# Optimization experiments

Measured on AMD Instinct MI355X. Metric: run time of the kernel, lower is better.

## Reference

```python
import jax, jax.numpy as jnp
import numpy as np

MAX_DISP = 64  # init kwarg max_disp; feature_similarity='correlation'


def setup_inputs() -> dict:
    key = jax.random.key(0)
    k1, k2 = jax.random.split(key)
    shape = (8, 160, 320, 128)  # (b, h, w, c)
    left = jax.random.normal(k1, shape, dtype=jnp.float32)
    right = jax.random.normal(k2, shape, dtype=jnp.float32)
    return {"left_feature": left, "right_feature": right}


def reference(left_feature, right_feature):
    # Faithful to CostVolume.__call__ with feature_similarity='correlation':
    # cost[b,h,j,i] = mean_c( left[b,h,j,c] * right[b,h,j-i,c] ) for j >= i, else 0.
    b, h, w, c = left_feature.shape
    widx = jnp.arange(w)  # (w,)
    slices = []
    for i in range(MAX_DISP):  # fixed hyperparameter unroll, not a data dim
        # roll brings right[..., j-i, :] to position j along width; wrapped
        # positions j < i are masked to zero (original leaves them at init 0).
        corr = jnp.mean(left_feature * jnp.roll(right_feature, i, axis=2), axis=3)  # (b,h,w)
        corr = jnp.where(widx >= i, corr, jnp.zeros((), corr.dtype))
        slices.append(corr)
    return jnp.stack(slices, axis=-1)  # (b, h, w, max_disp)
```

## Files before the change

### kernel.cpp

```cpp
#include <hip/hip_runtime.h>

#define W  320
#define TJ 64

typedef __attribute__((ext_vector_type(8))) short   short8;
typedef __attribute__((ext_vector_type(4))) float   floatx4;

__device__ __forceinline__ unsigned int f2bf(float f) {
    unsigned int u = __float_as_uint(f);
    u += 0x7FFFu + ((u >> 16) & 1u);
    return u >> 16;
}

__global__ __launch_bounds__(512, 8)
void cost_volume_kernel(const float* __restrict__ Lg,
                        const float* __restrict__ Rg,
                        float* __restrict__ out) {
    __shared__ unsigned short S[128 * 128];

    const int lin  = blockIdx.x;
    const int work = (lin & 7) * 800 + (lin >> 3);
    const int bh   = work / 5;
    const int jt   = work - bh * 5;
    const int j0   = jt * TJ;
    const int tid  = threadIdx.x;

    const int lr    = tid >> 5;
    const int half  = tid & 1;
    const int chunk = (tid & 31) >> 1;
    const int cf    = (tid & 31) << 2;

    const int wave = tid >> 6;
    const int lane = tid & 63;
    const int col  = lane & 15;
    const int quad = lane >> 4;
    const int mt   = wave >> 1;
    const int g    = wave & 1;
    const int m0   = mt * 16;
    const int ntb  = mt + g * 3;
    const int NT   = g ? 2 : 3;

    const float* Rrow0 = Rg + (size_t)(bh * W) * 128;
    #pragma unroll
    for (int p = 0; p < 8; ++p) {
        const int rr = p * 16 + lr;
        const int k  = j0 - 63 + rr;
        floatx4 v;
        v.x = 0.f; v.y = 0.f; v.z = 0.f; v.w = 0.f;
        if (k >= 0 && k < W) v = *(const floatx4*)(Rrow0 + (size_t)k * 128 + cf);
        uint2 d;
        d.x = f2bf(v.x) | (f2bf(v.y) << 16);
        d.y = f2bf(v.z) | (f2bf(v.w) << 16);
        const int sw = chunk ^ (rr & 15);
        *(uint2*)&S[rr * 128 + (sw << 3) + half * 4] = d;
    }

    const float* Arow = Lg + (size_t)(bh * W + j0 + m0 + col) * 128 + quad * 8;
    short8 af[4];
    #pragma unroll
    for (int ks = 0; ks < 4; ++ks) {
        floatx4 lo = *(const floatx4*)(Arow + ks * 32);
        floatx4 hi = *(const floatx4*)(Arow + ks * 32 + 4);
        short8 a;
        a[0] = (short)f2bf(lo.x); a[1] = (short)f2bf(lo.y);
        a[2] = (short)f2bf(lo.z); a[3] = (short)f2bf(lo.w);
        a[4] = (short)f2bf(hi.x); a[5] = (short)f2bf(hi.y);
        a[6] = (short)f2bf(hi.z); a[7] = (short)f2bf(hi.w);
        af[ks] = a;
    }

    __syncthreads();

    floatx4 acc[3];
    #pragma unroll
    for (int t = 0; t < 3; ++t) { acc[t].x = 0.f; acc[t].y = 0.f; acc[t].z = 0.f; acc[t].w = 0.f; }

    #pragma unroll
    for (int ks = 0; ks < 4; ++ks) {
        const int sc = (ks * 4 + quad) ^ col;
        #pragma unroll
        for (int t = 0; t < 3; ++t) {
            if (t < NT) {
                const int nrow = (ntb + t) * 16 + col;
                const short8 bf = *(const short8*)&S[nrow * 128 + (sc << 3)];
                acc[t] = __builtin_amdgcn_mfma_f32_16x16x32_bf16(af[ks], bf, acc[t], 0, 0, 0);
            }
        }
    }

    float* obase = out + (size_t)(bh * W + j0) * 64;
    #pragma unroll
    for (int t = 0; t < 3; ++t) {
        if (t < NT) {
            const int n = (ntb + t) * 16 + col;
            #pragma unroll
            for (int r = 0; r < 4; ++r) {
                const int m = m0 + quad * 4 + r;
                const int i = m + 63 - n;
                if (i >= 0 && i < 64) {
                    obase[m * 64 + i] = acc[t][r] * 0.0078125f;
                }
            }
        }
    }
}

extern "C" void kernel_launch(void* const* d_in, const int* in_sizes, int n_in,
                              void* d_out, int out_size, void* d_ws, size_t ws_size,
                              hipStream_t stream) {
    const float* L = (const float*)d_in[0];
    const float* R = (const float*)d_in[1];
    float* out = (float*)d_out;
    dim3 grid(8 * 160 * (W / TJ));
    cost_volume_kernel<<<grid, 512, 0, stream>>>(L, R, out);
}
```

Baseline: 445.0 us.

## Process a whole image row per block, staging the full right row in LDS

Each workgroup now covers one entire (b,h) row instead of a 64-column tile. It loads all 320 right-feature rows into LDS as bf16 once, then 10 waves each handle two 16-row left tiles against a 5-tile disparity band. This removes the 63-row halo re-read and per-tile zero padding of right features, so global reads of R drop by about half. In exchange it uses about 80KB of LDS per block, launches only 1280 larger blocks and lowers occupancy, which could leave latency less hidden.

New measurement: 432.0 us. 1.03x faster.

```diff
diff --git a/kernel.cpp b/kernel.cpp
--- a/kernel.cpp
+++ b/kernel.cpp
@@ -1,7 +1,6 @@
 #include <hip/hip_runtime.h>
 
-#define W  320
-#define TJ 64
+#define W 320
 
 typedef __attribute__((ext_vector_type(8))) short   short8;
 typedef __attribute__((ext_vector_type(4))) float   floatx4;
@@ -12,93 +11,90 @@
     return u >> 16;
 }
 
-__global__ __launch_bounds__(512, 8)
+__global__ __launch_bounds__(640, 5)
 void cost_volume_kernel(const float* __restrict__ Lg,
                         const float* __restrict__ Rg,
                         float* __restrict__ out) {
-    __shared__ unsigned short S[128 * 128];
+    __shared__ unsigned short S[W * 128];
 
-    const int lin  = blockIdx.x;
-    const int work = (lin & 7) * 800 + (lin >> 3);
-    const int bh   = work / 5;
-    const int jt   = work - bh * 5;
-    const int j0   = jt * TJ;
-    const int tid  = threadIdx.x;
+    const int bh  = blockIdx.x;
+    const int tid = threadIdx.x;
 
     const int lr    = tid >> 5;
     const int half  = tid & 1;
     const int chunk = (tid & 31) >> 1;
     const int cf    = (tid & 31) << 2;
 
+    const float* Rrow0 = Rg + (size_t)bh * W * 128;
+    #pragma unroll
+    for (int p = 0; p < 16; ++p) {
+        const int k = p * 20 + lr;
+        floatx4 v = *(const floatx4*)(Rrow0 + (size_t)k * 128 + cf);
+        uint2 d;
+        d.x = f2bf(v.x) | (f2bf(v.y) << 16);
+        d.y = f2bf(v.z) | (f2bf(v.w) << 16);
+        const int sw = chunk ^ (k & 15);
+        *(uint2*)&S[k * 128 + (sw << 3) + half * 4] = d;
+    }
+
+    __syncthreads();
+
     const int wave = tid >> 6;
     const int lane = tid & 63;
     const int col  = lane & 15;
     const int quad = lane >> 4;
-    const int mt   = wave >> 1;
-    const int g    = wave & 1;
-    const int m0   = mt * 16;
-    const int ntb  = mt + g * 3;
-    const int NT   = g ? 2 : 3;
 
-    const float* Rrow0 = Rg + (size_t)(bh * W) * 128;
-    #pragma unroll
-    for (int p = 0; p < 8; ++p) {
-        const int rr = p * 16 + lr;
-        const int k  = j0 - 63 + rr;
-        floatx4 v;
-        v.x = 0.f; v.y = 0.f; v.z = 0.f; v.w = 0.f;
-        if (k >= 0 && k < W) v = *(const floatx4*)(Rrow0 + (size_t)k * 128 + cf);
-        uint2 d;
-        d.x = f2bf(v.x) | (f2bf(v.y) << 16);
-        d.y = f2bf(v.z) | (f2bf(v.w) << 16);
-        const int sw = chunk ^ (rr & 15);
-        *(uint2*)&S[rr * 128 + (sw << 3) + half * 4] = d;
-    }
-
-    const float* Arow = Lg + (size_t)(bh * W + j0 + m0 + col) * 128 + quad * 8;
-    short8 af[4];
-    #pragma unroll
-    for (int ks = 0; ks < 4; ++ks) {
-        floatx4 lo = *(const floatx4*)(Arow + ks * 32);
-        floatx4 hi = *(const floatx4*)(Arow + ks * 32 + 4);
-        short8 a;
-        a[0] = (short)f2bf(lo.x); a[1] = (short)f2bf(lo.y);
-        a[2] = (short)f2bf(lo.z); a[3] = (short)f2bf(lo.w);
-        a[4] = (short)f2bf(hi.x); a[5] = (short)f2bf(hi.y);
-        a[6] = (short)f2bf(hi.z); a[7] = (short)f2bf(hi.w);
-        af[ks] = a;
-    }
-
-    __syncthreads();
-
-    floatx4 acc[3];
-    #pragma unroll
-    for (int t = 0; t < 3; ++t) { acc[t].x = 0.f; acc[t].y = 0.f; acc[t].z = 0.f; acc[t].w = 0.f; }
+    const float* Lrow0 = Lg + (size_t)bh * W * 128;
+    float* obase = out + (size_t)bh * W * 64;
 
     #pragma unroll
-    for (int ks = 0; ks < 4; ++ks) {
-        const int sc = (ks * 4 + quad) ^ col;
+    for (int s = 0; s < 2; ++s) {
+        const int mt = wave + s * 10;
+        const int m0 = mt * 16;
+
+        const float* Arow = Lrow0 + (size_t)(m0 + col) * 128 + quad * 8;
+        short8 af[4];
         #pragma unroll
-        for (int t = 0; t < 3; ++t) {
-            if (t < NT) {
-                const int nrow = (ntb + t) * 16 + col;
-                const short8 bf = *(const short8*)&S[nrow * 128 + (sc << 3)];
-                acc[t] = __builtin_amdgcn_mfma_f32_16x16x32_bf16(af[ks], bf, acc[t], 0, 0, 0);
+        for (int ks = 0; ks < 4; ++ks) {
+            floatx4 lo = *(const floatx4*)(Arow + ks * 32);
+            floatx4 hi = *(const floatx4*)(Arow + ks * 32 + 4);
+            short8 a;
+            a[0] = (short)f2bf(lo.x); a[1] = (short)f2bf(lo.y);
+            a[2] = (short)f2bf(lo.z); a[3] = (short)f2bf(lo.w);
+            a[4] = (short)f2bf(hi.x); a[5] = (short)f2bf(hi.y);
+            a[6] = (short)f2bf(hi.z); a[7] = (short)f2bf(hi.w);
+            af[ks] = a;
+        }
+
+        floatx4 acc[5];
+        #pragma unroll
+        for (int t = 0; t < 5; ++t) {
+            acc[t].x = 0.f; acc[t].y = 0.f; acc[t].z = 0.f; acc[t].w = 0.f;
+        }
+
+        const int kbase = m0 - 64;
+        #pragma unroll
+        for (int t = 0; t < 5; ++t) {
+            const int kt = kbase + t * 16;
+            if (kt >= 0) {
+                const int krow = kt + col;
+                #pragma unroll
+                for (int ks = 0; ks < 4; ++ks) {
+                    const int sc = (ks * 4 + quad) ^ col;
+                    const short8 bf = *(const short8*)&S[krow * 128 + (sc << 3)];
+                    acc[t] = __builtin_amdgcn_mfma_f32_16x16x32_bf16(af[ks], bf, acc[t], 0, 0, 0);
+                }
             }
         }
-    }
 
-    float* obase = out + (size_t)(bh * W + j0) * 64;
-    #pragma unroll
-    for (int t = 0; t < 3; ++t) {
-        if (t < NT) {
-            const int n = (ntb + t) * 16 + col;
+        #pragma unroll
+        for (int t = 0; t < 5; ++t) {
             #pragma unroll
             for (int r = 0; r < 4; ++r) {
-                const int m = m0 + quad * 4 + r;
-                const int i = m + 63 - n;
+                const int m = quad * 4 + r;
+                const int i = 64 + m - t * 16 - col;
                 if (i >= 0 && i < 64) {
-                    obase[m * 64 + i] = acc[t][r] * 0.0078125f;
+                    obase[(size_t)(m0 + m) * 64 + i] = acc[t][r] * 0.0078125f;
                 }
             }
         }
@@ -111,6 +107,6 @@
     const float* L = (const float*)d_in[0];
     const float* R = (const float*)d_in[1];
     float* out = (float*)d_out;
-    dim3 grid(8 * 160 * (W / TJ));
-    cost_volume_kernel<<<grid, 512, 0, stream>>>(L, R, out);
+    dim3 grid(8 * 160);
+    cost_volume_kernel<<<grid, 640, 0, stream>>>(L, R, out);
 }
```
